# Kernel tuning notes

Measured on AMD Instinct MI355X. Metric: run time of the kernel, lower is better.

## Reference

```python
import jax, jax.numpy as jnp
import numpy as np

EPS = 1e-12


def _update_side(states, left, right, layer_idx, cache_position):
    """Norm-based rank decomposition scatter update for one of K or V.

    states: [H, S, D] float32 (batch dim already squeezed)
    left:   [L, H, M, R] float16 cache buffer
    right:  [L, H, R, D] float16 cache buffer
    Semantics match the torch loop: for each head h and each position i,
      left[layer, h, pos_i, 0] = ||states[h, i]||_2, left[layer, h, pos_i, 1:] = 0
      right[layer, h]          = zeros; row 0 = normalized states of the LAST i
    (right is overwritten every iteration, so only the last position survives).
    Returns (reconstructed [1, S, ...], new_left, new_right).
    Assumes cache_position == arange(S) starting from an empty cache, so
    current_seq_len == S (static shape, jit-friendly).
    """
    H, S, D = states.shape
    R = left.shape[-1]
    # per-position L2 norms -> first rank column, rest zero
    norms = jnp.linalg.norm(states, axis=-1)                      # [H, S]
    rows = jnp.zeros((H, S, R), left.dtype).at[:, :, 0].set(norms.astype(left.dtype))
    left_layer = left[layer_idx].at[:, cache_position, :].set(rows)   # [H, M, R]
    left = left.at[layer_idx].set(left_layer)
    last = states[:, -1, :]                                       # [H, D]
    last_n = last / (jnp.linalg.norm(last, axis=-1, keepdims=True) + EPS)
    right_layer = jnp.zeros((H, R, D), right.dtype).at[:, 0, :].set(last_n.astype(right.dtype))
    right = right.at[layer_idx].set(right_layer)
    # reconstruction in fp32 over the filled prefix (current_seq_len == S)
    recon = jnp.einsum(
        'hsr,hrd->hsd',
        left[layer_idx][:, :S, :].astype(jnp.float32),
        right[layer_idx].astype(jnp.float32),
    )
    return recon[None], left, right  # [1, H, S, D]


def setup_inputs() -> dict:
    key = jax.random.key(0)
    k0, k1 = jax.random.split(key)
    L, H, M, R, D, S = 8, 32, 8192, 16, 128, 4096
    return {
        'key_states': jax.random.normal(k0, (1, H, S, D), jnp.float32),
        'value_states': jax.random.normal(k1, (1, H, S, D), jnp.float32),
        'k_left': jnp.zeros((L, H, M, R), jnp.float16),
        'k_right': jnp.zeros((L, H, R, D), jnp.float16),
        'v_left': jnp.zeros((L, H, M, R), jnp.float16),
        'v_right': jnp.zeros((L, H, R, D), jnp.float16),
        'cache_position': jnp.arange(S, dtype=jnp.int32),
        'layer_idx': 3,
    }


def reference(key_states, value_states, k_left, k_right, v_left, v_right,
              cache_position, layer_idx):
    k_full, _, _ = _update_side(key_states[0], k_left, k_right, layer_idx, cache_position)
    v_full, _, _ = _update_side(value_states[0], v_left, v_right, layer_idx, cache_position)
    return k_full, v_full
```

## Files before the change

### kernel.cpp

```cpp
#include <hip/hip_runtime.h>
#include <hip/hip_fp16.h>

constexpr int H = 32;
constexpr int S = 4096;
constexpr int D = 128;
constexpr float EPSF = 1e-12f;

typedef float vfloat4 __attribute__((ext_vector_type(4)));

__global__ void VLKV_lastn_kernel(const float* __restrict__ K,
                                  const float* __restrict__ V,
                                  float* __restrict__ lastn) {
    const int bid  = blockIdx.x;
    const int side = bid >> 5;
    const int lane = threadIdx.x;
    const int h    = bid & (H - 1);
    const float* src = (side == 0 ? K : V) + ((size_t)h * S + (S - 1)) * D;

    float2 v = *(const float2*)(src + lane * 2);
    float ss = v.x * v.x + v.y * v.y;
#pragma unroll
    for (int m = 1; m < 64; m <<= 1) ss += __shfl_xor(ss, m);
    const float inv = 1.0f / (sqrtf(ss) + EPSF);

    float2 o;
    o.x = __half2float(__float2half(v.x * inv));
    o.y = __half2float(__float2half(v.y * inv));
    *(float2*)(lastn + (size_t)bid * D + lane * 2) = o;
}

__global__ void VLKV_recon_kernel(const float* __restrict__ K,
                                  const float* __restrict__ V,
                                  const float* __restrict__ lastn,
                                  float* __restrict__ out) {
    const int tid  = threadIdx.x;
    const int lane = tid & 63;
    const int wv   = tid >> 6;
    const int half = lane >> 5;
    const int li   = lane & 31;
    const int wpb  = blockDim.x >> 6;

    const long nwaves = (long)gridDim.x * wpb;
    const long npairs = (long)H * S;

    for (long rp = (long)blockIdx.x * wpb + wv; rp < npairs; rp += nwaves) {
        const long row  = rp * 2 + half;
        const int  side = (int)(row >> 17);
        const long srow = row & (long)(H * S - 1);

        const float* src = (side == 0 ? K : V) + srow * (long)D + li * 4;
        const float4 x = *(const float4*)src;
        float ss = x.x * x.x + x.y * x.y + x.z * x.z + x.w * x.w;
#pragma unroll
        for (int m = 1; m < 32; m <<= 1) ss += __shfl_xor(ss, m);

        const float nh = __half2float(__float2half(sqrtf(ss)));

        const float4 ln = *(const float4*)(lastn + (row >> 12) * (long)D + li * 4);

        vfloat4 o;
        o.x = nh * ln.x;
        o.y = nh * ln.y;
        o.z = nh * ln.z;
        o.w = nh * ln.w;
        __builtin_nontemporal_store(o, (vfloat4*)(out + row * (long)D + li * 4));
    }
}

extern "C" void kernel_launch(void* const* d_in, const int* in_sizes, int n_in,
                              void* d_out, int out_size, void* d_ws, size_t ws_size,
                              hipStream_t stream) {
    const float* K = (const float*)d_in[0];
    const float* V = (const float*)d_in[1];
    float* out   = (float*)d_out;
    float* lastn = (float*)d_ws;

    VLKV_lastn_kernel<<<2 * H, 64, 0, stream>>>(K, V, lastn);
    VLKV_recon_kernel<<<2048, 256, 0, stream>>>(K, V, lastn, out);
}
```

Measured before the change: 52.06 us.

## Fuse last-row normalization into reconstruction kernel and assign contiguous row chunks per wave

Removes the separate lastn kernel and its workspace round trip. Each wave now recomputes the normalized last row for its head in registers and then processes a fixed contiguous chunk of 32 rows, replacing the grid-stride loop. This saves a kernel launch and the dependency between the two kernels. In exchange, every wave performs one redundant 512-byte load and normalization, and the grid size is now tied exactly to the problem size.

```diff
diff --git a/kernel.cpp b/kernel.cpp
--- a/kernel.cpp
+++ b/kernel.cpp
@@ -8,62 +8,51 @@
 
 typedef float vfloat4 __attribute__((ext_vector_type(4)));
 
-__global__ void VLKV_lastn_kernel(const float* __restrict__ K,
+__global__ void VLKV_fused_kernel(const float* __restrict__ K,
                                   const float* __restrict__ V,
-                                  float* __restrict__ lastn) {
-    const int bid  = blockIdx.x;
-    const int side = bid >> 5;
-    const int lane = threadIdx.x;
-    const int h    = bid & (H - 1);
-    const float* src = (side == 0 ? K : V) + ((size_t)h * S + (S - 1)) * D;
-
-    float2 v = *(const float2*)(src + lane * 2);
-    float ss = v.x * v.x + v.y * v.y;
-#pragma unroll
-    for (int m = 1; m < 64; m <<= 1) ss += __shfl_xor(ss, m);
-    const float inv = 1.0f / (sqrtf(ss) + EPSF);
-
-    float2 o;
-    o.x = __half2float(__float2half(v.x * inv));
-    o.y = __half2float(__float2half(v.y * inv));
-    *(float2*)(lastn + (size_t)bid * D + lane * 2) = o;
-}
-
-__global__ void VLKV_recon_kernel(const float* __restrict__ K,
-                                  const float* __restrict__ V,
-                                  const float* __restrict__ lastn,
                                   float* __restrict__ out) {
     const int tid  = threadIdx.x;
     const int lane = tid & 63;
     const int wv   = tid >> 6;
     const int half = lane >> 5;
     const int li   = lane & 31;
-    const int wpb  = blockDim.x >> 6;
 
-    const long nwaves = (long)gridDim.x * wpb;
-    const long npairs = (long)H * S;
+    const long w    = (long)blockIdx.x * (blockDim.x >> 6) + wv;
+    const long row0 = w * 32;
+    const int  side = (int)(row0 >> 17);
+    const long srow0 = row0 & (long)(H * S - 1);
+    const int  h    = (int)(srow0 >> 12);
 
-    for (long rp = (long)blockIdx.x * wpb + wv; rp < npairs; rp += nwaves) {
-        const long row  = rp * 2 + half;
-        const int  side = (int)(row >> 17);
-        const long srow = row & (long)(H * S - 1);
+    const float* base = (side == 0 ? K : V);
 
-        const float* src = (side == 0 ? K : V) + srow * (long)D + li * 4;
-        const float4 x = *(const float4*)src;
+    const float4 lv = *(const float4*)(base + ((long)h * S + (S - 1)) * D + li * 4);
+    float lss = lv.x * lv.x + lv.y * lv.y + lv.z * lv.z + lv.w * lv.w;
+#pragma unroll
+    for (int m = 1; m < 32; m <<= 1) lss += __shfl_xor(lss, m);
+    const float inv = 1.0f / (sqrtf(lss) + EPSF);
+    float4 ln;
+    ln.x = __half2float(__float2half(lv.x * inv));
+    ln.y = __half2float(__float2half(lv.y * inv));
+    ln.z = __half2float(__float2half(lv.z * inv));
+    ln.w = __half2float(__float2half(lv.w * inv));
+
+    const float* src = base + (srow0 + half) * (long)D + li * 4;
+    float*       dst = out  + (row0  + half) * (long)D + li * 4;
+
+#pragma unroll 4
+    for (int i = 0; i < 16; ++i) {
+        const float4 x = *(const float4*)(src + (long)i * 2 * D);
         float ss = x.x * x.x + x.y * x.y + x.z * x.z + x.w * x.w;
 #pragma unroll
         for (int m = 1; m < 32; m <<= 1) ss += __shfl_xor(ss, m);
-
         const float nh = __half2float(__float2half(sqrtf(ss)));
-
-        const float4 ln = *(const float4*)(lastn + (row >> 12) * (long)D + li * 4);
 
         vfloat4 o;
         o.x = nh * ln.x;
         o.y = nh * ln.y;
         o.z = nh * ln.z;
         o.w = nh * ln.w;
-        __builtin_nontemporal_store(o, (vfloat4*)(out + row * (long)D + li * 4));
+        __builtin_nontemporal_store(o, (vfloat4*)(dst + (long)i * 2 * D));
     }
 }
 
@@ -72,9 +61,7 @@
                               hipStream_t stream) {
     const float* K = (const float*)d_in[0];
     const float* V = (const float*)d_in[1];
-    float* out   = (float*)d_out;
-    float* lastn = (float*)d_ws;
+    float* out = (float*)d_out;
 
-    VLKV_lastn_kernel<<<2 * H, 64, 0, stream>>>(K, V, lastn);
-    VLKV_recon_kernel<<<2048, 256, 0, stream>>>(K, V, lastn, out);
+    VLKV_fused_kernel<<<2048, 256, 0, stream>>>(K, V, out);
 }
```

Result: faster. 44.81 us (-13.9%).
